# Kernel optimization log

Measured on AMD Instinct MI355X. Metric: run time of the kernel, lower is better.

Reference implementation:

```python
import jax, jax.numpy as jnp
import numpy as np

TOKEN_SELF_ATTN_VALUE = -5e4  # reformer_pytorch constant for masking self-attention
BUCKET_SIZE = 64
N_HASHES = 4
HEADS = 8


def look_one_back(x):
    # concat each chunk with the previous chunk along the within-chunk axis (axis=2)
    prev = jnp.concatenate([x[:, -1:], x[:, :-1]], axis=1)
    return jnp.concatenate([prev, x], axis=2)


def lsh_attention(qk, v, rotations):
    # qk, v: (b*h, t, dh); rotations: (dh, n_hashes, n_buckets//2)
    bh, seqlen, dim = qk.shape
    n_buckets = seqlen // BUCKET_SIZE
    # --- LSH bucket hashing via random rotations ---
    rotated = jnp.einsum('btf,fhi->bhti', qk, rotations)            # (bh, H, t, nb/2)
    rotated = jnp.concatenate([rotated, -rotated], axis=-1)          # (bh, H, t, nb)
    buckets = jnp.argmax(rotated, axis=-1)                           # (bh, H, t)
    offsets = (jnp.arange(N_HASHES) * n_buckets)[None, :, None]
    buckets = (buckets + offsets).reshape(bh, N_HASHES * seqlen)
    # --- stable sort tokens by (bucket, position) ---
    ticker = jnp.arange(N_HASHES * seqlen)
    buckets_and_t = seqlen * buckets + (ticker % seqlen)[None, :]
    sticker = jnp.argsort(buckets_and_t, axis=-1)                    # sorted ticker
    undo_sort = jnp.argsort(sticker, axis=-1)
    st = sticker % seqlen                                            # original positions
    sqk = jnp.take_along_axis(qk, st[..., None], axis=1)
    sv = jnp.take_along_axis(v, st[..., None], axis=1)
    # --- chunk into n_hashes*n_buckets chunks of bucket_size tokens ---
    n_chunks = N_HASHES * n_buckets
    bq_t = st.reshape(bh, n_chunks, -1)
    bqk = sqk.reshape(bh, n_chunks, -1, dim)
    bv = sv.reshape(bh, n_chunks, -1, dim)
    bq = bqk
    bk = bqk / jnp.maximum(jnp.linalg.norm(bqk, axis=-1, keepdims=True), 1e-12)
    bk = look_one_back(bk)
    bv = look_one_back(bv)
    bkv_t = look_one_back(bq_t)
    # --- chunked attention with one-chunk lookback ---
    dots = jnp.einsum('bcie,bcje->bcij', bq, bk) * (dim ** -0.5)     # (bh, nc, bs, 2*bs)
    dots = jnp.where(bq_t[:, :, :, None] == bkv_t[:, :, None, :], TOKEN_SELF_ATTN_VALUE, dots)
    dots_lse = jax.nn.logsumexp(dots, axis=-1, keepdims=True)
    probs = jnp.exp(dots - dots_lse)
    bo = jnp.einsum('bcij,bcje->bcie', probs, bv)
    so = bo.reshape(bh, N_HASHES * seqlen, dim)
    slogits = dots_lse.reshape(bh, N_HASHES * seqlen)
    # --- unsort and combine hash rounds weighted by logsumexp ---
    o = jnp.take_along_axis(so, undo_sort[..., None], axis=1)
    logits = jnp.take_along_axis(slogits, undo_sort, axis=1)
    o = o.reshape(bh, N_HASHES, seqlen, dim)
    logits = logits.reshape(bh, N_HASHES, seqlen, 1)
    w = jnp.exp(logits - jax.nn.logsumexp(logits, axis=1, keepdims=True))
    return jnp.sum(o * w, axis=1)


def _forward(queries, Wqk, Wv, Wo, bo, rotations):
    B, N, C = queries.shape
    m = BUCKET_SIZE * 2
    if N % m != 0:  # fit_length: zero-pad to multiple of bucket_size*2 (static)
        pad = m - N % m
        x = jnp.concatenate([queries, jnp.zeros((B, pad, C), queries.dtype)], axis=1)
    else:
        x = queries
    T = x.shape[1]
    dh = C // HEADS
    qk = jnp.einsum('btc,cf->btf', x, Wqk).reshape(B, T, HEADS, dh).transpose(0, 2, 1, 3).reshape(B * HEADS, T, dh)
    v = jnp.einsum('btc,cf->btf', x, Wv).reshape(B, T, HEADS, dh).transpose(0, 2, 1, 3).reshape(B * HEADS, T, dh)
    out = lsh_attention(qk, v, rotations)
    out = out.reshape(B, HEADS, T, dh).transpose(0, 2, 1, 3).reshape(B, T, C)
    out = jnp.einsum('btc,cf->btf', out, Wo) + bo
    return out[:, :N]


def setup_inputs() -> dict:
    key = jax.random.key(0)
    ks = jax.random.split(key, 7)
    B, N, C = 4, 4096, 512
    dh = C // HEADS
    n_buckets = N // BUCKET_SIZE  # 64
    return {
        'queries': jax.random.normal(ks[0], (B, N, C), jnp.float32),
        'keys': jax.random.normal(ks[1], (B, N, C), jnp.float32),
        'values': jax.random.normal(ks[2], (B, N, C), jnp.float32),
        'attn_mask': jnp.zeros((1,), jnp.bool_),
        'tau': 1,
        'delta': 1,
        'Wqk': jax.random.normal(ks[3], (C, C), jnp.float32) / np.float32(np.sqrt(C)),
        'Wv': jax.random.normal(ks[4], (C, C), jnp.float32) / np.float32(np.sqrt(C)),
        'Wo': jax.random.normal(ks[5], (C, C), jnp.float32) / np.float32(np.sqrt(C)),
        'bo': jnp.zeros((C,), jnp.float32),
        'rotations': jax.random.normal(ks[6], (dh, N_HASHES, n_buckets // 2), jnp.float32),
    }


def reference(queries, keys, values, attn_mask, tau, delta, Wqk, Wv, Wo, bo, rotations):
    # keys/values/attn_mask/tau/delta are accepted but unused, matching the torch module
    return _forward(queries, Wqk, Wv, Wo, bo, rotations)
```

## Files before the change

### kernel.cpp

```cpp
#include <hip/hip_runtime.h>
#include <hip/hip_bf16.h>
#include <cstdint>
#include <cstddef>

#define LSEQ   4096
#define DHD    64
#define NHASH  4
#define CDIM   512
#define NBH    32
#define MROWS  16384
#define NCHUNK 256

typedef __attribute__((ext_vector_type(8))) short short8;
typedef __attribute__((ext_vector_type(4))) float f32x4;
typedef __attribute__((ext_vector_type(2))) float f32x2;

__device__ inline uint32_t f2bf(float f) {
  uint32_t u = __float_as_uint(f);
  return (u + 0x7FFFu + ((u >> 16) & 1u)) >> 16;
}
__device__ inline float bf2f(uint32_t h) { return __uint_as_float(h << 16); }
__device__ inline void split2(float f, uint32_t& hi, uint32_t& lo) {
  hi = f2bf(f);
  lo = f2bf(f - bf2f(hi));
}
__device__ inline uint32_t cvtpk_bf16(float a, float b) {
  uint32_t r;
  asm("v_cvt_pk_bf16_f32 %0, %1, %2" : "=v"(r) : "v"(a), "v"(b));
  return r;
}
__device__ inline short8 ldsK(const uint16_t* p) {
  union { uint2 u[2]; short8 s; } t;
  t.u[0] = *reinterpret_cast<const uint2*>(p);
  t.u[1] = *reinterpret_cast<const uint2*>(p + 4);
  return t.s;
}

__global__ __launch_bounds__(256) void prep_kernel(
    const float* __restrict__ Wv, const float* __restrict__ Wo,
    uint16_t* __restrict__ wvT0, uint16_t* __restrict__ wvT1,
    uint16_t* __restrict__ woT_hi, uint16_t* __restrict__ woT_lo)
{
  __shared__ float Ts[32][33];
  const int bid = blockIdx.x, tid = threadIdx.x;
  if (bid < 1024) {
    int idx = bid * 256 + tid;
    int k = idx >> 9, n = idx & 511;
    uint32_t hi, lo;
    split2(Wo[idx], hi, lo);
    woT_hi[n * 512 + k] = (uint16_t)hi;
    woT_lo[n * 512 + k] = (uint16_t)lo;
  } else {
    int wb = bid - 1024;
    const int k0 = (wb >> 4) * 32, n0 = (wb & 15) * 32;
#pragma unroll
    for (int i = 0; i < 4; i++) {
      int flat = i * 256 + tid;
      int r = flat >> 5, c = flat & 31;
      Ts[r][c] = Wv[(size_t)(k0 + r) * 512 + n0 + c];
    }
    __syncthreads();
#pragma unroll
    for (int i = 0; i < 4; i++) {
      int flat = i * 256 + tid;
      int nr = flat >> 5, kc = flat & 31;
      uint32_t h, l;
      split2(Ts[kc][nr], h, l);
      size_t idx = (size_t)(n0 + nr) * 512 + k0 + kc;
      wvT0[idx] = (uint16_t)h;
      wvT1[idx] = (uint16_t)l;
    }
  }
}

__global__ __launch_bounds__(512) void gemm_qk_kernel(
    const float* __restrict__ X, const float* __restrict__ Wqk,
    float* __restrict__ qk, uint16_t* __restrict__ qkhi,
    uint16_t* __restrict__ qklo, float* __restrict__ invn_g)
{
  const int m0 = blockIdx.x * 128;
  const int n0 = blockIdx.y * 128;
  __shared__ float As[32][132];
  __shared__ float Bs[32][132];
  const int tid = threadIdx.x;
  const int r = tid >> 5, c = tid & 31;
  f32x2 acc2[8][2];
#pragma unroll
  for (int i = 0; i < 8; i++) {
    acc2[i][0] = {0.f, 0.f};
    acc2[i][1] = {0.f, 0.f};
  }

  const int arow = tid >> 2;
  const int ak   = (tid & 3) * 4;
  const int brow = tid >> 4;
  const int bn   = (tid & 15) * 4;

  float4 pa[2], pb[2];
#pragma unroll
  for (int rr = 0; rr < 2; rr++) {
    pa[rr] = *reinterpret_cast<const float4*>(&X[(size_t)(m0 + arow) * CDIM + ak + rr * 16]);
    pb[rr] = *reinterpret_cast<const float4*>(&Wqk[(size_t)brow * CDIM + n0 + bn + rr * 64]);
  }

  for (int kb = 0; kb < CDIM; kb += 32) {
#pragma unroll
    for (int rr = 0; rr < 2; rr++) {
      As[ak + rr * 16 + 0][arow] = pa[rr].x;
      As[ak + rr * 16 + 1][arow] = pa[rr].y;
      As[ak + rr * 16 + 2][arow] = pa[rr].z;
      As[ak + rr * 16 + 3][arow] = pa[rr].w;
      *reinterpret_cast<float4*>(&Bs[brow][bn + rr * 64]) = pb[rr];
    }
    __syncthreads();
    if (kb + 32 < CDIM) {
#pragma unroll
      for (int rr = 0; rr < 2; rr++) {
        pa[rr] = *reinterpret_cast<const float4*>(
            &X[(size_t)(m0 + arow) * CDIM + kb + 32 + ak + rr * 16]);
        pb[rr] = *reinterpret_cast<const float4*>(
            &Wqk[(size_t)(kb + 32 + brow) * CDIM + n0 + bn + rr * 64]);
      }
    }
#pragma unroll
    for (int k = 0; k < 32; k++) {
      float4 a0 = *reinterpret_cast<const float4*>(&As[k][r * 8]);
      float4 a1 = *reinterpret_cast<const float4*>(&As[k][r * 8 + 4]);
      float4 b  = *reinterpret_cast<const float4*>(&Bs[k][c * 4]);
      float am[8] = {a0.x, a0.y, a0.z, a0.w, a1.x, a1.y, a1.z, a1.w};
      f32x2 b01 = {b.x, b.y};
      f32x2 b23 = {b.z, b.w};
#pragma unroll
      for (int i = 0; i < 8; i++) {
        f32x2 av = {am[i], am[i]};
        acc2[i][0] += av * b01;
        acc2[i][1] += av * b23;
      }
    }
    __syncthreads();
  }
  const int head = (n0 >> 6) + (c >> 4);
#pragma unroll
  for (int ii = 0; ii < 8; ii++) {
    int m = m0 + r * 8 + ii;
    int b = m >> 12, t = m & 4095;
    size_t base = ((size_t)(b * 8 + head) * LSEQ + t) * DHD + (c & 15) * 4;
    float4 ov = {acc2[ii][0][0], acc2[ii][0][1], acc2[ii][1][0], acc2[ii][1][1]};
    *reinterpret_cast<float4*>(&qk[base]) = ov;
    uint32_t h0 = cvtpk_bf16(ov.x, ov.y);
    uint32_t h1 = cvtpk_bf16(ov.z, ov.w);
    float r0 = ov.x - __uint_as_float(h0 << 16);
    float r1 = ov.y - __uint_as_float(h0 & 0xffff0000u);
    float r2 = ov.z - __uint_as_float(h1 << 16);
    float r3 = ov.w - __uint_as_float(h1 & 0xffff0000u);
    *reinterpret_cast<uint2*>(&qkhi[base]) = {h0, h1};
    *reinterpret_cast<uint2*>(&qklo[base]) = {cvtpk_bf16(r0, r1), cvtpk_bf16(r2, r3)};
    float ss = ov.x * ov.x + ov.y * ov.y + ov.z * ov.z + ov.w * ov.w;
    ss += __shfl_xor(ss, 1, 64);
    ss += __shfl_xor(ss, 2, 64);
    ss += __shfl_xor(ss, 4, 64);
    ss += __shfl_xor(ss, 8, 64);
    if ((c & 15) == 0)
      invn_g[(size_t)(b * 8 + head) * LSEQ + t] = 1.0f / fmaxf(sqrtf(ss), 1e-12f);
  }
}

__global__ __launch_bounds__(512) void gemm_v_mfma_kernel(
    const float* __restrict__ Xf,
    const uint16_t* __restrict__ Wv0, const uint16_t* __restrict__ Wv1,
    uint16_t* __restrict__ vhi)
{
  __shared__ __align__(16) uint16_t Xs[2 * 128 * 40];
  __shared__ __align__(16) uint16_t Ws[2 * 128 * 40];
  const int tid = threadIdx.x;
  const int m0 = blockIdx.x * 128;
  const int n0 = blockIdx.y * 128;
  const int lane = tid & 63, w = tid >> 6;
  const int l16 = lane & 15, lg = lane >> 4;

  f32x4 acc[8];
#pragma unroll
  for (int nt = 0; nt < 8; nt++) acc[nt] = {0.f, 0.f, 0.f, 0.f};

  const int srow = tid >> 3;
  const int sch = (tid & 7) * 4;

  for (int kb = 0; kb < CDIM; kb += 32) {
#pragma unroll
    for (int i = 0; i < 2; i++) {
      int row = i * 64 + srow;
      float4 v = *reinterpret_cast<const float4*>(
          &Xf[(size_t)(m0 + row) * CDIM + kb + sch]);
      uint32_t h01 = cvtpk_bf16(v.x, v.y);
      uint32_t h23 = cvtpk_bf16(v.z, v.w);
      float r0 = v.x - __uint_as_float(h01 << 16);
      float r1 = v.y - __uint_as_float(h01 & 0xffff0000u);
      float r2 = v.z - __uint_as_float(h23 << 16);
      float r3 = v.w - __uint_as_float(h23 & 0xffff0000u);
      uint2 hw = {h01, h23};
      uint2 lw = {cvtpk_bf16(r0, r1), cvtpk_bf16(r2, r3)};
      *reinterpret_cast<uint2*>(Xs + row * 40 + sch) = hw;
      *reinterpret_cast<uint2*>(Xs + 5120 + row * 40 + sch) = lw;
    }
#pragma unroll
    for (int i = 0; i < 4; i++) {
      int p = i >> 1;
      int row = (i & 1) * 64 + srow;
      const uint16_t* wg = (p == 0) ? Wv0 : Wv1;
      *reinterpret_cast<uint2*>(Ws + p * 5120 + row * 40 + sch) =
          *reinterpret_cast<const uint2*>(wg + (size_t)(n0 + row) * 512 + kb + sch);
    }
    __syncthreads();

    const int abase = (w * 16 + l16) * 40 + lg * 8;
    short8 a0 = *reinterpret_cast<const short8*>(Xs + abase);
    short8 a1 = *reinterpret_cast<const short8*>(Xs + 5120 + abase);
#pragma unroll
    for (int nt = 0; nt < 8; nt++) {
      int bbase = (nt * 16 + l16) * 40 + lg * 8;
      short8 b0 = *reinterpret_cast<const short8*>(Ws + bbase);
      short8 b1 = *reinterpret_cast<const short8*>(Ws + 5120 + bbase);
      acc[nt] = __builtin_amdgcn_mfma_f32_16x16x32_bf16(a0, b0, acc[nt], 0, 0, 0);
      acc[nt] = __builtin_amdgcn_mfma_f32_16x16x32_bf16(a1, b0, acc[nt], 0, 0, 0);
      acc[nt] = __builtin_amdgcn_mfma_f32_16x16x32_bf16(a0, b1, acc[nt], 0, 0, 0);
    }
    __syncthreads();
  }

#pragma unroll
  for (int rr = 0; rr < 4; rr++) {
    int mg = m0 + w * 16 + lg * 4 + rr;
    int b = mg >> 12, t = mg & 4095;
#pragma unroll
    for (int nt = 0; nt < 8; nt++) {
      int head = (n0 >> 6) + (nt >> 2);
      size_t base = ((size_t)(b * 8 + head) * LSEQ + t) * DHD + (nt & 3) * 16 + l16;
      vhi[base] = (uint16_t)cvtpk_bf16(acc[nt][rr], acc[nt][rr]);
    }
  }
}

__global__ __launch_bounds__(256) void hash_kernel(
    const float* __restrict__ qk, const float* __restrict__ rot,
    int* __restrict__ buckets)
{
  __shared__ float rotT[128][68];
  const int tid = threadIdx.x;
  for (int idx = tid; idx < 64 * 128; idx += 256) {
    int f = idx >> 7, hi = idx & 127;
    rotT[hi][f] = rot[idx];
  }
  __syncthreads();
  const int bh = blockIdx.y;
  const int t = blockIdx.x * 256 + tid;
  float4 row4[16];
  const float* src = &qk[((size_t)bh * LSEQ + t) * DHD];
#pragma unroll
  for (int i = 0; i < 16; i++) row4[i] = reinterpret_cast<const float4*>(src)[i];

  int* bout = &buckets[(size_t)bh * NHASH * LSEQ];
  for (int h = 0; h < NHASH; h++) {
    float rc[32];
    float best = -3.0e38f;
    int bidx = 0;
#pragma unroll 4
    for (int i = 0; i < 32; i++) {
      const float* rr = &rotT[h * 32 + i][0];
      float a = 0.f;
#pragma unroll
      for (int f4 = 0; f4 < 16; f4++) {
        float4 rv = reinterpret_cast<const float4*>(rr)[f4];
        a += row4[f4].x * rv.x + row4[f4].y * rv.y + row4[f4].z * rv.z + row4[f4].w * rv.w;
      }
      rc[i] = a;
      if (a > best) { best = a; bidx = i; }
    }
#pragma unroll
    for (int i = 0; i < 32; i++) {
      float nv = -rc[i];
      if (nv > best) { best = nv; bidx = 32 + i; }
    }
    bout[h * LSEQ + t] = bidx;
  }
}

__global__ __launch_bounds__(256) void sort_kernel(
    const int* __restrict__ buckets, int* __restrict__ st)
{
  __shared__ int hist[64][64];
  const int h = blockIdx.x, bh = blockIdx.y;
  const int tid = threadIdx.x;
  const int* bk = &buckets[((size_t)bh * NHASH + h) * LSEQ];

  for (int i = tid; i < 64 * 64; i += 256) (&hist[0][0])[i] = 0;
  __syncthreads();
  for (int t = tid; t < LSEQ; t += 256) {
    int b = bk[t];
    atomicAdd(&hist[t >> 6][b], 1);
  }
  __syncthreads();
  if (tid < 64) {
    int tot = 0;
    for (int s = 0; s < 64; s++) tot += hist[s][tid];
    int vsc = tot;
    for (int off = 1; off < 64; off <<= 1) {
      int nv = __shfl_up(vsc, off, 64);
      if (tid >= off) vsc += nv;
    }
    int run = h * LSEQ + (vsc - tot);
    for (int s = 0; s < 64; s++) {
      int tmp = hist[s][tid];
      hist[s][tid] = run;
      run += tmp;
    }
  }
  __syncthreads();
  const int wave = tid >> 6, lane = tid & 63;
  const uint64_t below = (lane == 63) ? 0x7fffffffffffffffull
                                      : ((1ull << lane) - 1ull);
  for (int si = 0; si < 16; si++) {
    int seg = wave * 16 + si;
    int pos = seg * 64 + lane;
    int b = bk[pos];
    uint64_t same = ~0ull;
#pragma unroll
    for (int j = 0; j < 6; j++) {
      uint64_t bal = __ballot((b >> j) & 1);
      same &= ((b >> j) & 1) ? bal : ~bal;
    }
    int rank = __popcll(same & below);
    int dest = hist[seg][b] + rank;
    st[(size_t)bh * (NHASH * LSEQ) + dest] = pos;
  }
}

__global__ __launch_bounds__(256) void attn_kernel(
    const uint16_t* __restrict__ qkhi, const uint16_t* __restrict__ qklo,
    const uint16_t* __restrict__ vhi, const float* __restrict__ invn_g,
    const int* __restrict__ st, uint16_t* __restrict__ o,
    float* __restrict__ lse_out)
{
  __shared__ __align__(16) uint8_t smem[53248];
  uint16_t* Khi  = (uint16_t*)smem;
  uint16_t* Klo  = Khi + 128 * 68;
  uint16_t* Vthi = (uint16_t*)(smem + 34816);
  float*    invn = (float*)(smem + 52224);
  int*      kpos = (int*)(smem + 52736);
  uint32_t* P32  = (uint32_t*)smem;

  const int lin = blockIdx.y * 256 + blockIdx.x;
  const int xcd = lin & 7, sidx = lin >> 3;
  const int bh = (xcd << 2) | (sidx >> 8);
  const int cchunk = sidx & 255;

  const int tid = threadIdx.x;
  const int prev = (cchunk + NCHUNK - 1) & (NCHUNK - 1);
  const int* stb = &st[(size_t)bh * (NHASH * LSEQ)];
  const int h = cchunk >> 6;

  if (tid < 128) {
    int kp = (tid < 64) ? stb[prev * 64 + tid] : stb[cchunk * 64 + (tid - 64)];
    kpos[tid] = kp;
    invn[tid] = invn_g[(size_t)bh * LSEQ + kp];
  }
  __syncthreads();

  {
    const int d4 = tid & 15, rbase = tid >> 4;
    const uint16_t* qhb = qkhi + (size_t)bh * LSEQ * DHD;
    const uint16_t* qlb = qklo + (size_t)bh * LSEQ * DHD;
#pragma unroll
    for (int it = 0; it < 8; it++) {
      int row = rbase + it * 16;
      size_t src = (size_t)kpos[row] * DHD + d4 * 4;
      *reinterpret_cast<uint2*>(Khi + row * 68 + d4 * 4) =
          *reinterpret_cast<const uint2*>(qhb + src);
      *reinterpret_cast<uint2*>(Klo + row * 68 + d4 * 4) =
          *reinterpret_cast<const uint2*>(qlb + src);
    }
  }
  {
    const int d4 = tid & 15, jg0 = tid >> 4;
    const uint16_t* vb = vhi + (size_t)bh * LSEQ * DHD;
#pragma unroll
    for (int half = 0; half < 2; half++) {
      int jg = jg0 + half * 16;
      uint2 vr[4];
#pragma unroll
      for (int s = 0; s < 4; s++)
        vr[s] = *reinterpret_cast<const uint2*>(vb + (size_t)kpos[jg * 4 + s] * DHD + d4 * 4);
#pragma unroll
      for (int i = 0; i < 4; i++) {
        int d = d4 * 4 + i;
        uint32_t e0 = (((i & 2) ? vr[0].y : vr[0].x) >> ((i & 1) * 16)) & 0xffffu;
        uint32_t e1 = (((i & 2) ? vr[1].y : vr[1].x) >> ((i & 1) * 16)) & 0xffffu;
        uint32_t e2 = (((i & 2) ? vr[2].y : vr[2].x) >> ((i & 1) * 16)) & 0xffffu;
        uint32_t e3 = (((i & 2) ? vr[3].y : vr[3].x) >> ((i & 1) * 16)) & 0xffffu;
        uint2 outw = {e0 | (e1 << 16), e2 | (e3 << 16)};
        int cpr = (jg >> 1) ^ (d & 15);
        *reinterpret_cast<uint2*>(Vthi + d * 128 + cpr * 8 + (jg & 1) * 4) = outw;
      }
    }
  }
  __syncthreads();

  const int lane = tid & 63, w = tid >> 6;
  const int l16 = lane & 15, lg = lane >> 4;

  f32x4 acc[8];
#pragma unroll
  for (int nt = 0; nt < 8; nt++) acc[nt] = {0.f, 0.f, 0.f, 0.f};

  __builtin_amdgcn_s_setprio(1);
#pragma unroll
  for (int ks = 0; ks < 2; ks++) {
    int aoff = (64 + w * 16 + l16) * 68 + ks * 32 + lg * 8;
    short8 a_hi = ldsK(Khi + aoff);
    short8 a_lo = ldsK(Klo + aoff);
#pragma unroll
    for (int nt = 0; nt < 8; nt++) {
      int boff = (nt * 16 + l16) * 68 + ks * 32 + lg * 8;
      short8 b_hi = ldsK(Khi + boff);
      short8 b_lo = ldsK(Klo + boff);
      acc[nt] = __builtin_amdgcn_mfma_f32_16x16x32_bf16(a_hi, b_hi, acc[nt], 0, 0, 0);
      acc[nt] = __builtin_amdgcn_mfma_f32_16x16x32_bf16(a_lo, b_hi, acc[nt], 0, 0, 0);
      acc[nt] = __builtin_amdgcn_mfma_f32_16x16x32_bf16(a_hi, b_lo, acc[nt], 0, 0, 0);
    }
  }
  __builtin_amdgcn_s_setprio(0);

  float invc[8]; int kpc[8];
#pragma unroll
  for (int nt = 0; nt < 8; nt++) {
    invc[nt] = invn[nt * 16 + l16] * 0.125f;
    kpc[nt] = kpos[nt * 16 + l16];
  }
  float pll[4];
#pragma unroll
  for (int r = 0; r < 4; r++) {
    int q = w * 16 + lg * 4 + r;
    int qp = kpos[64 + q];
    float mm = -3.0e38f;
#pragma unroll
    for (int nt = 0; nt < 8; nt++) {
      float s = acc[nt][r] * invc[nt];
      if (qp == kpc[nt]) s = -5e4f;
      acc[nt][r] = s;
      mm = fmaxf(mm, s);
    }
    mm = fmaxf(mm, __shfl_xor(mm, 1, 64));
    mm = fmaxf(mm, __shfl_xor(mm, 2, 64));
    mm = fmaxf(mm, __shfl_xor(mm, 4, 64));
    mm = fmaxf(mm, __shfl_xor(mm, 8, 64));
    float ll = 0.f;
#pragma unroll
    for (int nt = 0; nt < 8; nt++) {
      float p = __expf(acc[nt][r] - mm);
      acc[nt][r] = p;
      ll += p;
    }
    ll += __shfl_xor(ll, 1, 64);
    ll += __shfl_xor(ll, 2, 64);
    ll += __shfl_xor(ll, 4, 64);
    ll += __shfl_xor(ll, 8, 64);
    if (l16 == 0)
      lse_out[(size_t)bh * (NHASH * LSEQ) + h * LSEQ + qp] = mm + __logf(ll);
    pll[r] = 1.0f / ll;
  }
  __syncthreads();

#pragma unroll
  for (int r = 0; r < 4; r++) {
    int q = w * 16 + lg * 4 + r;
#pragma unroll
    for (int nt = 0; nt < 8; nt++) {
      float p = acc[nt][r];
      uint32_t t1 = cvtpk_bf16(p, p);
      float res = p - __uint_as_float(t1 << 16);
      P32[q * 132 + nt * 16 + l16] = cvtpk_bf16(p, res);
    }
  }

  f32x4 oacc[4];
#pragma unroll
  for (int nt = 0; nt < 4; nt++) oacc[nt] = {0.f, 0.f, 0.f, 0.f};

  __builtin_amdgcn_s_setprio(1);
#pragma unroll
  for (int ks = 0; ks < 4; ks++) {
    const uint32_t* pr = P32 + (w * 16 + l16) * 132 + ks * 32 + lg * 8;
    uint4 ua = *reinterpret_cast<const uint4*>(pr);
    uint4 ub = *reinterpret_cast<const uint4*>(pr + 4);
    uint32_t u[8] = {ua.x, ua.y, ua.z, ua.w, ub.x, ub.y, ub.z, ub.w};
    union { uint32_t w4[4]; short8 s8; } ph, pl;
#pragma unroll
    for (int k2 = 0; k2 < 4; k2++) {
      ph.w4[k2] = (u[2 * k2] & 0xffffu) | (u[2 * k2 + 1] << 16);
      pl.w4[k2] = (u[2 * k2] >> 16) | (u[2 * k2 + 1] & 0xffff0000u);
    }
    const int cc = ks * 4 + lg;
#pragma unroll
    for (int nt = 0; nt < 4; nt++) {
      int voff = (nt * 16 + l16) * 128 + ((cc ^ l16) & 15) * 8;
      short8 v_hi = *reinterpret_cast<const short8*>(Vthi + voff);
      oacc[nt] = __builtin_amdgcn_mfma_f32_16x16x32_bf16(ph.s8, v_hi, oacc[nt], 0, 0, 0);
      oacc[nt] = __builtin_amdgcn_mfma_f32_16x16x32_bf16(pl.s8, v_hi, oacc[nt], 0, 0, 0);
    }
  }
  __builtin_amdgcn_s_setprio(0);

  {
    uint16_t* ob = o + ((size_t)bh * (NHASH * LSEQ) + (size_t)h * LSEQ) * DHD;
#pragma unroll
    for (int r = 0; r < 4; r++) {
      int q = w * 16 + lg * 4 + r;
      int qp = kpos[64 + q];
      float s = pll[r];
#pragma unroll
      for (int nt = 0; nt < 4; nt++) {
        float v = oacc[nt][r] * s;
        ob[(size_t)qp * DHD + nt * 16 + l16] = (uint16_t)cvtpk_bf16(v, v);
      }
    }
  }
}

__global__ __launch_bounds__(256) void combine_kernel(
    const uint16_t* __restrict__ o, const float* __restrict__ lse,
    uint16_t* __restrict__ comb_hi, uint16_t* __restrict__ comb_lo)
{
  int gid = blockIdx.x * 4 + (threadIdx.x >> 6);
  int lane = threadIdx.x & 63;
  int bh = gid >> 12;
  int pos = gid & 4095;
  const float* lb = &lse[(size_t)bh * (NHASH * LSEQ) + pos];
  float l0 = lb[0], l1 = lb[LSEQ], l2 = lb[2 * LSEQ], l3 = lb[3 * LSEQ];
  float m = fmaxf(fmaxf(l0, l1), fmaxf(l2, l3));
  float w0 = __expf(l0 - m), w1 = __expf(l1 - m), w2 = __expf(l2 - m), w3 = __expf(l3 - m);
  float inv = 1.0f / (w0 + w1 + w2 + w3);
  const uint16_t* ob = &o[((size_t)bh * (NHASH * LSEQ) + pos) * DHD];
  float val = (w0 * bf2f(ob[lane]) + w1 * bf2f(ob[(size_t)LSEQ * DHD + lane]) +
               w2 * bf2f(ob[(size_t)2 * LSEQ * DHD + lane]) +
               w3 * bf2f(ob[(size_t)3 * LSEQ * DHD + lane])) * inv;
  int b = bh >> 3, head = bh & 7;
  size_t idx = ((size_t)(b * LSEQ + pos)) * CDIM + head * DHD + lane;
  uint32_t hw = cvtpk_bf16(val, val);
  float res = val - __uint_as_float(hw << 16);
  comb_hi[idx] = (uint16_t)hw;
  comb_lo[idx] = (uint16_t)cvtpk_bf16(res, res);
}

__global__ __launch_bounds__(512) void gemm_out_kernel(
    const uint16_t* __restrict__ Ahi_g, const uint16_t* __restrict__ Alo_g,
    const uint16_t* __restrict__ Bhi_g, const uint16_t* __restrict__ Blo_g,
    const float* __restrict__ bias, float* __restrict__ out)
{
  __shared__ __align__(16) uint16_t Ah[128 * 40];
  __shared__ __align__(16) uint16_t Al[128 * 40];
  __shared__ __align__(16) uint16_t Bh[128 * 40];
  __shared__ __align__(16) uint16_t Bl[128 * 40];
  const int tid = threadIdx.x;
  const int m0 = blockIdx.x * 128, n0 = blockIdx.y * 128;
  const int lane = tid & 63, w = tid >> 6;
  const int l16 = lane & 15, lg = lane >> 4;

  f32x4 acc[8];
#pragma unroll
  for (int nt = 0; nt < 8; nt++) acc[nt] = {0.f, 0.f, 0.f, 0.f};

  const int srow = tid >> 2;
  const int sch  = (tid & 3) * 8;

  for (int kb = 0; kb < CDIM; kb += 32) {
    *reinterpret_cast<uint4*>(Ah + srow * 40 + sch) =
        *reinterpret_cast<const uint4*>(Ahi_g + (size_t)(m0 + srow) * CDIM + kb + sch);
    *reinterpret_cast<uint4*>(Al + srow * 40 + sch) =
        *reinterpret_cast<const uint4*>(Alo_g + (size_t)(m0 + srow) * CDIM + kb + sch);
    *reinterpret_cast<uint4*>(Bh + srow * 40 + sch) =
        *reinterpret_cast<const uint4*>(Bhi_g + (size_t)(n0 + srow) * CDIM + kb + sch);
    *reinterpret_cast<uint4*>(Bl + srow * 40 + sch) =
        *reinterpret_cast<const uint4*>(Blo_g + (size_t)(n0 + srow) * CDIM + kb + sch);
    __syncthreads();

    const int abase = (w * 16 + l16) * 40 + lg * 8;
    short8 ah = *reinterpret_cast<const short8*>(Ah + abase);
    short8 al = *reinterpret_cast<const short8*>(Al + abase);
#pragma unroll
    for (int nt = 0; nt < 8; nt++) {
      int bbase = (nt * 16 + l16) * 40 + lg * 8;
      short8 bh_ = *reinterpret_cast<const short8*>(Bh + bbase);
      short8 bl_ = *reinterpret_cast<const short8*>(Bl + bbase);
      acc[nt] = __builtin_amdgcn_mfma_f32_16x16x32_bf16(ah, bh_, acc[nt], 0, 0, 0);
      acc[nt] = __builtin_amdgcn_mfma_f32_16x16x32_bf16(al, bh_, acc[nt], 0, 0, 0);
      acc[nt] = __builtin_amdgcn_mfma_f32_16x16x32_bf16(ah, bl_, acc[nt], 0, 0, 0);
    }
    __syncthreads();
  }
#pragma unroll
  for (int nt = 0; nt < 8; nt++) {
    int n = n0 + nt * 16 + l16;
    float bv = bias[n];
#pragma unroll
    for (int rr = 0; rr < 4; rr++) {
      int mg = m0 + w * 16 + lg * 4 + rr;
      out[(size_t)mg * CDIM + n] = acc[nt][rr] + bv;
    }
  }
}

extern "C" void kernel_launch(void* const* d_in, const int* in_sizes, int n_in,
                              void* d_out, int out_size, void* d_ws, size_t ws_size,
                              hipStream_t stream) {
  (void)in_sizes; (void)n_in; (void)out_size; (void)ws_size;
  const float* X    = (const float*)d_in[0];
  const float* Wqk  = (const float*)d_in[6];
  const float* Wv   = (const float*)d_in[7];
  const float* Wo   = (const float*)d_in[8];
  const float* bo   = (const float*)d_in[9];
  const float* rot  = (const float*)d_in[10];

  uint8_t* W = (uint8_t*)d_ws;
  float*    qk      = (float*)(W + 0);
  uint16_t* obuf    = (uint16_t*)(W + 33554432);
  uint16_t* qkhi    = (uint16_t*)(W + 100663296);
  uint16_t* qklo    = (uint16_t*)(W + 117440512);
  uint16_t* vhi     = (uint16_t*)(W + 134217728);
  int*      buckets = (int*)(W + 150994944);
  int*      st      = (int*)(W + 153092096);
  float*    lse     = (float*)(W + 155189248);
  float*    invn_g  = (float*)(W + 157286400);
  uint16_t* woT_hi  = (uint16_t*)(W + 157810688);
  uint16_t* woT_lo  = (uint16_t*)(W + 158334976);
  uint16_t* wvT0    = (uint16_t*)(W + 158859264);
  uint16_t* wvT1    = (uint16_t*)(W + 159383552);
  uint16_t* comb_hi = (uint16_t*)(W + 0);
  uint16_t* comb_lo = (uint16_t*)(W + 16777216);

  hipLaunchKernelGGL(prep_kernel, dim3(1280), dim3(256), 0, stream,
                     Wv, Wo, wvT0, wvT1, woT_hi, woT_lo);
  hipLaunchKernelGGL(gemm_qk_kernel, dim3(128, 4), dim3(512), 0, stream,
                     X, Wqk, qk, qkhi, qklo, invn_g);
  hipLaunchKernelGGL(gemm_v_mfma_kernel, dim3(128, 4), dim3(512), 0, stream,
                     X, wvT0, wvT1, vhi);
  hipLaunchKernelGGL(hash_kernel, dim3(16, 32), dim3(256), 0, stream,
                     qk, rot, buckets);
  hipLaunchKernelGGL(sort_kernel, dim3(4, 32), dim3(256), 0, stream,
                     buckets, st);
  hipLaunchKernelGGL(attn_kernel, dim3(256, 32), dim3(256), 0, stream,
                     qkhi, qklo, vhi, invn_g, st, obuf, lse);
  hipLaunchKernelGGL(combine_kernel, dim3(32768), dim3(256), 0, stream,
                     obuf, lse, comb_hi, comb_lo);
  hipLaunchKernelGGL(gemm_out_kernel, dim3(128, 4), dim3(512), 0, stream,
                     comb_hi, comb_lo, woT_hi, woT_lo, bo, (float*)d_out);
}
```

Before: 415.6 us.

## Load QK low parts from global, drop split-bf16 for probabilities in PV

The attention kernel no longer stages the low bf16 half of K in LDS. It reads the low parts straight from global memory into registers for the QK matmul, which shrinks LDS use and may raise occupancy. The probability matrix is now stored as a single bf16 instead of a hi/lo pair, halving the PV MFMAs and dropping the unpacking work. The trade-off is lower PV precision and uncoalesced global gathers in the inner loop.

```diff
diff --git a/kernel.cpp b/kernel.cpp
--- a/kernel.cpp
+++ b/kernel.cpp
@@ -340,13 +340,12 @@
     const int* __restrict__ st, uint16_t* __restrict__ o,
     float* __restrict__ lse_out)
 {
-  __shared__ __align__(16) uint8_t smem[53248];
+  __shared__ __align__(16) uint8_t smem[34816];
   uint16_t* Khi  = (uint16_t*)smem;
-  uint16_t* Klo  = Khi + 128 * 68;
-  uint16_t* Vthi = (uint16_t*)(smem + 34816);
-  float*    invn = (float*)(smem + 52224);
-  int*      kpos = (int*)(smem + 52736);
-  uint32_t* P32  = (uint32_t*)smem;
+  uint16_t* Vthi = (uint16_t*)(smem + 17408);
+  float*    invn = (float*)(smem + 33792);
+  int*      kpos = (int*)(smem + 34304);
+  uint16_t* P16  = (uint16_t*)smem;
 
   const int lin = blockIdx.y * 256 + blockIdx.x;
   const int xcd = lin & 7, sidx = lin >> 3;
@@ -368,15 +367,12 @@
   {
     const int d4 = tid & 15, rbase = tid >> 4;
     const uint16_t* qhb = qkhi + (size_t)bh * LSEQ * DHD;
-    const uint16_t* qlb = qklo + (size_t)bh * LSEQ * DHD;
 #pragma unroll
     for (int it = 0; it < 8; it++) {
       int row = rbase + it * 16;
       size_t src = (size_t)kpos[row] * DHD + d4 * 4;
       *reinterpret_cast<uint2*>(Khi + row * 68 + d4 * 4) =
           *reinterpret_cast<const uint2*>(qhb + src);
-      *reinterpret_cast<uint2*>(Klo + row * 68 + d4 * 4) =
-          *reinterpret_cast<const uint2*>(qlb + src);
     }
   }
   {
@@ -407,6 +403,15 @@
   const int lane = tid & 63, w = tid >> 6;
   const int l16 = lane & 15, lg = lane >> 4;
 
+  float invc[8]; int kpc[8];
+#pragma unroll
+  for (int nt = 0; nt < 8; nt++) {
+    invc[nt] = invn[nt * 16 + l16] * 0.125f;
+    kpc[nt] = kpos[nt * 16 + l16];
+  }
+  const int qp_a = kpos[64 + w * 16 + l16];
+  const uint16_t* qlb = qklo + (size_t)bh * LSEQ * DHD;
+
   f32x4 acc[8];
 #pragma unroll
   for (int nt = 0; nt < 8; nt++) acc[nt] = {0.f, 0.f, 0.f, 0.f};
@@ -416,25 +421,24 @@
   for (int ks = 0; ks < 2; ks++) {
     int aoff = (64 + w * 16 + l16) * 68 + ks * 32 + lg * 8;
     short8 a_hi = ldsK(Khi + aoff);
-    short8 a_lo = ldsK(Klo + aoff);
+    short8 a_lo = *reinterpret_cast<const short8*>(
+        qlb + (size_t)qp_a * DHD + ks * 32 + lg * 8);
+    short8 blo[8];
+#pragma unroll
+    for (int nt = 0; nt < 8; nt++)
+      blo[nt] = *reinterpret_cast<const short8*>(
+          qlb + (size_t)kpc[nt] * DHD + ks * 32 + lg * 8);
 #pragma unroll
     for (int nt = 0; nt < 8; nt++) {
       int boff = (nt * 16 + l16) * 68 + ks * 32 + lg * 8;
       short8 b_hi = ldsK(Khi + boff);
-      short8 b_lo = ldsK(Klo + boff);
       acc[nt] = __builtin_amdgcn_mfma_f32_16x16x32_bf16(a_hi, b_hi, acc[nt], 0, 0, 0);
       acc[nt] = __builtin_amdgcn_mfma_f32_16x16x32_bf16(a_lo, b_hi, acc[nt], 0, 0, 0);
-      acc[nt] = __builtin_amdgcn_mfma_f32_16x16x32_bf16(a_hi, b_lo, acc[nt], 0, 0, 0);
+      acc[nt] = __builtin_amdgcn_mfma_f32_16x16x32_bf16(a_hi, blo[nt], acc[nt], 0, 0, 0);
     }
   }
   __builtin_amdgcn_s_setprio(0);
 
-  float invc[8]; int kpc[8];
-#pragma unroll
-  for (int nt = 0; nt < 8; nt++) {
-    invc[nt] = invn[nt * 16 + l16] * 0.125f;
-    kpc[nt] = kpos[nt * 16 + l16];
-  }
   float pll[4];
 #pragma unroll
   for (int r = 0; r < 4; r++) {
@@ -475,9 +479,7 @@
 #pragma unroll
     for (int nt = 0; nt < 8; nt++) {
       float p = acc[nt][r];
-      uint32_t t1 = cvtpk_bf16(p, p);
-      float res = p - __uint_as_float(t1 << 16);
-      P32[q * 132 + nt * 16 + l16] = cvtpk_bf16(p, res);
+      P16[q * 132 + nt * 16 + l16] = (uint16_t)cvtpk_bf16(p, p);
     }
   }
 
@@ -488,23 +490,14 @@
   __builtin_amdgcn_s_setprio(1);
 #pragma unroll
   for (int ks = 0; ks < 4; ks++) {
-    const uint32_t* pr = P32 + (w * 16 + l16) * 132 + ks * 32 + lg * 8;
-    uint4 ua = *reinterpret_cast<const uint4*>(pr);
-    uint4 ub = *reinterpret_cast<const uint4*>(pr + 4);
-    uint32_t u[8] = {ua.x, ua.y, ua.z, ua.w, ub.x, ub.y, ub.z, ub.w};
-    union { uint32_t w4[4]; short8 s8; } ph, pl;
-#pragma unroll
-    for (int k2 = 0; k2 < 4; k2++) {
-      ph.w4[k2] = (u[2 * k2] & 0xffffu) | (u[2 * k2 + 1] << 16);
-      pl.w4[k2] = (u[2 * k2] >> 16) | (u[2 * k2 + 1] & 0xffff0000u);
-    }
+    short8 pa = *reinterpret_cast<const short8*>(
+        P16 + (w * 16 + l16) * 132 + ks * 32 + lg * 8);
     const int cc = ks * 4 + lg;
 #pragma unroll
     for (int nt = 0; nt < 4; nt++) {
       int voff = (nt * 16 + l16) * 128 + ((cc ^ l16) & 15) * 8;
       short8 v_hi = *reinterpret_cast<const short8*>(Vthi + voff);
-      oacc[nt] = __builtin_amdgcn_mfma_f32_16x16x32_bf16(ph.s8, v_hi, oacc[nt], 0, 0, 0);
-      oacc[nt] = __builtin_amdgcn_mfma_f32_16x16x32_bf16(pl.s8, v_hi, oacc[nt], 0, 0, 0);
+      oacc[nt] = __builtin_amdgcn_mfma_f32_16x16x32_bf16(pa, v_hi, oacc[nt], 0, 0, 0);
     }
   }
   __builtin_amdgcn_s_setprio(0);
```

Measured after the change: 437.9 us. 1.05x slower.
